# Kernel optimization log

Hardware: AMD Instinct MI355X
Metric: run time of the kernel (lower is better)

The kernel has to match this reference:

```python
import jax, jax.numpy as jnp
import numpy as np

EPS = 1e-5

def _layernorm(x, w, b):
    mu = jnp.mean(x, axis=-1, keepdims=True)
    var = jnp.mean(jnp.square(x - mu), axis=-1, keepdims=True)
    return (x - mu) * jax.lax.rsqrt(var + EPS) * w + b

def setup_inputs() -> dict:
    key = jax.random.key(0)
    ks = jax.random.split(key, 8)
    L, D, FF = 4096, 768, 3072
    s = 1.0 / np.sqrt(D)
    return {
        "x": jax.random.normal(ks[0], (L, D), jnp.float32),
        "in_proj_w": jax.random.normal(ks[1], (3 * D, D), jnp.float32) * s,
        "in_proj_b": jnp.zeros((3 * D,), jnp.float32),
        "out_w": jax.random.normal(ks[2], (D, D), jnp.float32) * s,
        "out_b": jnp.zeros((D,), jnp.float32),
        "ln1_w": jnp.ones((D,), jnp.float32),
        "ln1_b": jnp.zeros((D,), jnp.float32),
        "ln2_w": jnp.ones((D,), jnp.float32),
        "ln2_b": jnp.zeros((D,), jnp.float32),
        "ff_w1": jax.random.normal(ks[3], (FF, D), jnp.float32) * s,
        "ff_b1": jnp.zeros((FF,), jnp.float32),
        "ff_w2": jax.random.normal(ks[4], (D, FF), jnp.float32) * (1.0 / np.sqrt(FF)),
        "ff_b2": jnp.zeros((D,), jnp.float32),
        "window": 128,
    }

def reference(x, in_proj_w, in_proj_b, out_w, out_b, ln1_w, ln1_b, ln2_w, ln2_b, ff_w1, ff_b1, ff_w2, ff_b2, window):
    L, D = x.shape
    H = 12
    hd = D // H
    # packed qkv projection (torch MultiheadAttention in_proj)
    qkv = x @ in_proj_w.T + in_proj_b          # [L, 3D]
    q, k, v = jnp.split(qkv, 3, axis=-1)
    q = q.reshape(L, H, hd).transpose(1, 0, 2)  # [H, L, hd]
    k = k.reshape(L, H, hd).transpose(1, 0, 2)
    v = v.reshape(L, H, hd).transpose(1, 0, 2)
    scores = jnp.einsum('hqd,hkd->hqk', q, k) / np.sqrt(hd)  # [H, L, L]
    idx = jnp.arange(L)
    banned = jnp.abs(idx[:, None] - idx[None, :]) > window    # True = disallowed
    scores = jnp.where(banned[None], -jnp.inf, scores)
    probs = jax.nn.softmax(scores, axis=-1)
    ctx = jnp.einsum('hqk,hkd->hqd', probs, v)               # [H, L, hd]
    ctx = ctx.transpose(1, 0, 2).reshape(L, D)
    attn_out = ctx @ out_w.T + out_b
    h = _layernorm(x + attn_out, ln1_w, ln1_b)
    ff = jax.nn.gelu(h @ ff_w1.T + ff_b1, approximate=False) @ ff_w2.T + ff_b2
    return _layernorm(h + ff, ln2_w, ln2_b)
```

## Files before the change

kernel.cpp:

```cpp
#include <hip/hip_runtime.h>

typedef __bf16 bf16x8 __attribute__((ext_vector_type(8)));
typedef float f32x4 __attribute__((ext_vector_type(4)));

__device__ __forceinline__ unsigned short f2b(float f) {
    unsigned int u = __float_as_uint(f);
    u = (u + 0x7fffu + ((u >> 16) & 1u)) >> 16;
    return (unsigned short)u;
}

__global__ __launch_bounds__(256) void cvt_all(
    const float* __restrict__ s0, unsigned short* __restrict__ d0,
    const float* __restrict__ s1, unsigned short* __restrict__ d1,
    const float* __restrict__ s2, unsigned short* __restrict__ d2,
    const float* __restrict__ s3, unsigned short* __restrict__ d3,
    const float* __restrict__ s4, unsigned short* __restrict__ d4)
{
    int i = blockIdx.x * 256 + threadIdx.x;
    const float* s; unsigned short* d; int j;
    if (i < 786432)       { s = s0; d = d0; j = i; }
    else if (i < 1228800) { s = s1; d = d1; j = i - 786432; }
    else if (i < 1376256) { s = s2; d = d2; j = i - 1228800; }
    else if (i < 1966080) { s = s3; d = d3; j = i - 1376256; }
    else                  { s = s4; d = d4; j = i - 1966080; }
    float4 v = ((const float4*)s)[j];
    ushort4 o;
    o.x = f2b(v.x); o.y = f2b(v.y); o.z = f2b(v.z); o.w = f2b(v.w);
    ((ushort4*)d)[j] = o;
}

#define GL16(g, s) __builtin_amdgcn_global_load_lds( \
    (const __attribute__((address_space(1))) unsigned int*)(g), \
    (__attribute__((address_space(3))) unsigned int*)(s), 16, 0, 0)

template<int EPI>
__global__ __launch_bounds__(512) void gemm_nt_256(
    const unsigned short* __restrict__ A,
    const unsigned short* __restrict__ B,
    const float* __restrict__ bias,
    float* __restrict__ Cf, unsigned short* __restrict__ Cb,
    int M, int N, int K)
{
    __shared__ __align__(16) unsigned short As[256 * 64];
    __shared__ __align__(16) unsigned short Bs[256 * 64];
    const int nwg = gridDim.x * gridDim.y;
    const int lin = blockIdx.y * gridDim.x + blockIdx.x;
    const int qq = nwg >> 3;
    const int swz = (lin & 7) * qq + (lin >> 3);
    const int bx = swz % gridDim.x;
    const int by = swz / gridDim.x;

    const int tid = threadIdx.x;
    const int l = tid & 63;
    const int w = tid >> 6;
    const int wr = w >> 2, wc = w & 3;
    const long arow = (long)by * 256 + (tid >> 3);
    const long brow = (long)bx * 256 + (tid >> 3);
    const int kc = (((tid & 7) ^ ((tid >> 3) & 7)) << 3);
    const unsigned short* Ap = A + arow * K + kc;
    const unsigned short* Bp = B + brow * K + kc;

    const int kslice = K / gridDim.z;
    const int kbeg = blockIdx.z * kslice;
    const int kend = kbeg + kslice;

    f32x4 acc[8][4] = {};

    for (int k0 = kbeg; k0 < kend; k0 += 64) {
#pragma unroll
        for (int i = 0; i < 4; ++i) {
            GL16(Ap + k0 + (long)64 * i * K, As + i * 4096 + tid * 8);
            GL16(Bp + k0 + (long)64 * i * K, Bs + i * 4096 + tid * 8);
        }
        __syncthreads();
#pragma unroll
        for (int kk = 0; kk < 2; ++kk) {
            bf16x8 b[4];
#pragma unroll
            for (int n = 0; n < 4; ++n) {
                const int row = wc * 64 + n * 16 + (l & 15);
                const int ch = (kk * 4 + (l >> 4)) ^ (row & 7);
                b[n] = *(const bf16x8*)&Bs[row * 64 + (ch << 3)];
            }
#pragma unroll
            for (int m = 0; m < 8; ++m) {
                const int row = wr * 128 + m * 16 + (l & 15);
                const int ch = (kk * 4 + (l >> 4)) ^ (row & 7);
                bf16x8 a = *(const bf16x8*)&As[row * 64 + (ch << 3)];
#pragma unroll
                for (int n = 0; n < 4; ++n)
                    acc[m][n] = __builtin_amdgcn_mfma_f32_16x16x32_bf16(a, b[n], acc[m][n], 0, 0, 0);
            }
        }
        __syncthreads();
    }

    const int r0 = by * 256 + wr * 128 + ((l >> 4) << 2);
    const int c0 = bx * 256 + wc * 64 + (l & 15);
#pragma unroll
    for (int n = 0; n < 4; ++n) {
        const int col = c0 + n * 16;
        const float bv = (EPI == 3) ? 0.0f : bias[col];
#pragma unroll
        for (int m = 0; m < 8; ++m) {
#pragma unroll
            for (int r = 0; r < 4; ++r) {
                long row = r0 + m * 16 + r;
                float v = acc[m][n][r];
                if (EPI == 3) {
                    Cf[(long)blockIdx.z * M * N + row * N + col] = v;
                } else {
                    v += bv;
                    if (EPI == 2) v = 0.5f * v * (1.0f + erff(v * 0.70710678f));
                    Cb[row * N + col] = f2b(v);
                }
            }
        }
    }
}

template<int EPI>
__global__ __launch_bounds__(256) void gemm_nt(
    const unsigned short* __restrict__ A,
    const unsigned short* __restrict__ B,
    const float* __restrict__ bias,
    float* __restrict__ Cf, unsigned short* __restrict__ Cb,
    int M, int N, int K)
{
    __shared__ __align__(16) unsigned short As[128 * 64];
    __shared__ __align__(16) unsigned short Bs[128 * 64];
    const int nwg = gridDim.x * gridDim.y;
    const int lin = blockIdx.y * gridDim.x + blockIdx.x;
    const int qq = nwg >> 3;
    const int swz = (lin & 7) * qq + (lin >> 3);
    const int bx = swz % gridDim.x;
    const int by = swz / gridDim.x;

    const int tid = threadIdx.x;
    const int l = tid & 63;
    const int w = tid >> 6;
    const int wr = w >> 1, wc = w & 1;
    const long arow = (long)by * 128 + (tid >> 3);
    const long brow = (long)bx * 128 + (tid >> 3);
    const int kc = (tid & 7) * 8;
    const unsigned short* Ap = A + arow * K + kc;
    const unsigned short* Bp = B + brow * K + kc;

    const int kslice = K / gridDim.z;
    const int kbeg = blockIdx.z * kslice;
    const int kend = kbeg + kslice;

    f32x4 acc[4][4] = {};

    for (int k0 = kbeg; k0 < kend; k0 += 64) {
#pragma unroll
        for (int i = 0; i < 4; ++i) {
            GL16(Ap + k0 + (long)32 * i * K, As + i * 2048 + tid * 8);
            GL16(Bp + k0 + (long)32 * i * K, Bs + i * 2048 + tid * 8);
        }
        __syncthreads();
#pragma unroll
        for (int kk = 0; kk < 2; ++kk) {
            bf16x8 a[4], b[4];
#pragma unroll
            for (int m = 0; m < 4; ++m)
                a[m] = *(const bf16x8*)&As[(wr * 64 + m * 16 + (l & 15)) * 64 + kk * 32 + (l >> 4) * 8];
#pragma unroll
            for (int n = 0; n < 4; ++n)
                b[n] = *(const bf16x8*)&Bs[(wc * 64 + n * 16 + (l & 15)) * 64 + kk * 32 + (l >> 4) * 8];
#pragma unroll
            for (int m = 0; m < 4; ++m)
#pragma unroll
                for (int n = 0; n < 4; ++n)
                    acc[m][n] = __builtin_amdgcn_mfma_f32_16x16x32_bf16(a[m], b[n], acc[m][n], 0, 0, 0);
        }
        __syncthreads();
    }

    const int r0 = by * 128 + wr * 64 + ((l >> 4) << 2);
    const int c0 = bx * 128 + wc * 64 + (l & 15);
#pragma unroll
    for (int n = 0; n < 4; ++n) {
        const int col = c0 + n * 16;
        const float bv = (EPI == 3) ? 0.0f : bias[col];
#pragma unroll
        for (int m = 0; m < 4; ++m) {
#pragma unroll
            for (int r = 0; r < 4; ++r) {
                long row = r0 + m * 16 + r;
                float v = acc[m][n][r];
                if (EPI == 3) {
                    Cf[(long)blockIdx.z * M * N + row * N + col] = v;
                } else {
                    v += bv;
                    if (EPI == 2) v = 0.5f * v * (1.0f + erff(v * 0.70710678f));
                    if (EPI == 1) Cf[row * N + col] = v;
                    else          Cb[row * N + col] = f2b(v);
                }
            }
        }
    }
}

__global__ __launch_bounds__(256) void attn_local(
    const unsigned short* __restrict__ qkv,
    unsigned short* __restrict__ ctx,
    const int* __restrict__ winp)
{
    const int L = 4096;
    const int W = *winp;
    const int h = blockIdx.y;
    const int q0 = blockIdx.x * 64;
    const int tid = threadIdx.x;
    const int w = tid >> 6, l = tid & 63;
    __shared__ __align__(16) unsigned short Qs[64 * 64];
    __shared__ __align__(16) unsigned short Ks[64 * 64];
    __shared__ __align__(16) unsigned short Vs[64 * 64];
    __shared__ __align__(16) unsigned short Ps[64 * 64];

    {
        const int cg = tid & 7;
#pragma unroll
        for (int i = 0; i < 2; ++i) {
            int r = (tid >> 3) + 32 * i;
            uint4 v = *(const uint4*)&qkv[(long)(q0 + r) * 2304 + h * 64 + cg * 8];
            *(uint4*)&Qs[r * 64 + ((cg ^ (r & 7)) << 3)] = v;
        }
    }

    float mrow[4], lrow[4];
    f32x4 o[4] = {};
#pragma unroll
    for (int r = 0; r < 4; ++r) { mrow[r] = -1e30f; lrow[r] = 0.0f; }

    for (int st = 0; st < 5; ++st) {
        const int k0 = q0 - 128 + st * 64;
        __syncthreads();
        {
            const int cg = tid & 7;
#pragma unroll
            for (int i = 0; i < 2; ++i) {
                int r = (tid >> 3) + 32 * i;
                int kr = k0 + r;
                int krc = kr < 0 ? 0 : (kr >= L ? L - 1 : kr);
                uint4 kv = *(const uint4*)&qkv[(long)krc * 2304 + 768 + h * 64 + cg * 8];
                *(uint4*)&Ks[r * 64 + ((cg ^ (r & 7)) << 3)] = kv;
                uint4 vv = *(const uint4*)&qkv[(long)krc * 2304 + 1536 + h * 64 + cg * 8];
#pragma unroll
                for (int jj = 0; jj < 4; ++jj) {
                    unsigned int word = (jj == 0) ? vv.x : (jj == 1) ? vv.y : (jj == 2) ? vv.z : vv.w;
                    int d0 = cg * 8 + jj * 2;
                    int d1 = d0 + 1;
                    Vs[d0 * 64 + (((r >> 3) ^ (d0 & 7)) << 3) + (r & 7)] = (unsigned short)(word & 0xffffu);
                    Vs[d1 * 64 + (((r >> 3) ^ (d1 & 7)) << 3) + (r & 7)] = (unsigned short)(word >> 16);
                }
            }
        }
        __syncthreads();

        f32x4 s[4] = {};
#pragma unroll
        for (int kk = 0; kk < 2; ++kk) {
            const int aro = w * 16 + (l & 15);
            bf16x8 aq = *(const bf16x8*)&Qs[aro * 64 + (((kk * 4 + (l >> 4)) ^ (aro & 7)) << 3)];
#pragma unroll
            for (int n = 0; n < 4; ++n) {
                const int bro = n * 16 + (l & 15);
                bf16x8 bk = *(const bf16x8*)&Ks[bro * 64 + (((kk * 4 + (l >> 4)) ^ (bro & 7)) << 3)];
                s[n] = __builtin_amdgcn_mfma_f32_16x16x32_bf16(aq, bk, s[n], 0, 0, 0);
            }
        }

        const int qrow = q0 + w * 16 + ((l >> 4) << 2);
        const int kcol = k0 + (l & 15);
        float p[4][4];
#pragma unroll
        for (int n = 0; n < 4; ++n) {
#pragma unroll
            for (int r = 0; r < 4; ++r) {
                int key = kcol + n * 16;
                int q = qrow + r;
                int dd = q - key; if (dd < 0) dd = -dd;
                bool banned = (key < 0) || (key >= L) || (dd > W);
                p[n][r] = banned ? -1e30f : s[n][r] * 0.125f;
            }
        }
        float mx[4];
#pragma unroll
        for (int r = 0; r < 4; ++r)
            mx[r] = fmaxf(fmaxf(p[0][r], p[1][r]), fmaxf(p[2][r], p[3][r]));
#pragma unroll
        for (int off = 8; off >= 1; off >>= 1)
#pragma unroll
            for (int r = 0; r < 4; ++r)
                mx[r] = fmaxf(mx[r], __shfl_xor(mx[r], off));

        float sc[4], mn[4];
#pragma unroll
        for (int r = 0; r < 4; ++r) {
            mn[r] = fmaxf(mrow[r], mx[r]);
            sc[r] = __expf(mrow[r] - mn[r]);
            mrow[r] = mn[r];
        }
        float rs[4] = {0.f, 0.f, 0.f, 0.f};
#pragma unroll
        for (int n = 0; n < 4; ++n)
#pragma unroll
            for (int r = 0; r < 4; ++r) {
                float pv = __expf(p[n][r] - mn[r]);
                p[n][r] = pv;
                rs[r] += pv;
            }
#pragma unroll
        for (int off = 8; off >= 1; off >>= 1)
#pragma unroll
            for (int r = 0; r < 4; ++r)
                rs[r] += __shfl_xor(rs[r], off);
#pragma unroll
        for (int r = 0; r < 4; ++r)
            lrow[r] = lrow[r] * sc[r] + rs[r];
#pragma unroll
        for (int n = 0; n < 4; ++n)
#pragma unroll
            for (int r = 0; r < 4; ++r)
                o[n][r] *= sc[r];

#pragma unroll
        for (int n = 0; n < 4; ++n) {
            int col = n * 16 + (l & 15);
            int cb = col >> 3, ci = col & 7;
#pragma unroll
            for (int r = 0; r < 4; ++r) {
                int rp = w * 16 + ((l >> 4) << 2) + r;
                Ps[rp * 64 + ((cb ^ (rp & 7)) << 3) + ci] = f2b(p[n][r]);
            }
        }
#pragma unroll
        for (int kk = 0; kk < 2; ++kk) {
            const int aro = w * 16 + (l & 15);
            bf16x8 ap = *(const bf16x8*)&Ps[aro * 64 + (((kk * 4 + (l >> 4)) ^ (aro & 7)) << 3)];
#pragma unroll
            for (int n = 0; n < 4; ++n) {
                const int bro = n * 16 + (l & 15);
                bf16x8 bv = *(const bf16x8*)&Vs[bro * 64 + (((kk * 4 + (l >> 4)) ^ (bro & 7)) << 3)];
                o[n] = __builtin_amdgcn_mfma_f32_16x16x32_bf16(ap, bv, o[n], 0, 0, 0);
            }
        }
    }

#pragma unroll
    for (int n = 0; n < 4; ++n) {
        int col = h * 64 + n * 16 + (l & 15);
#pragma unroll
        for (int r = 0; r < 4; ++r) {
            int q = q0 + w * 16 + ((l >> 4) << 2) + r;
            ctx[(long)q * 768 + col] = f2b(o[n][r] / lrow[r]);
        }
    }
}

__global__ __launch_bounds__(256) void ln_res2(
    const float* __restrict__ A, const float* __restrict__ parts,
    const float* __restrict__ pbias,
    const float* __restrict__ w, const float* __restrict__ bb,
    float* __restrict__ outf, unsigned short* __restrict__ outb)
{
    const int D = 768;
    const long PS = (long)4096 * 768;
    const int row = blockIdx.x;
    const int t = threadIdx.x;
    const long base = (long)row * D;
    float xs[3];
#pragma unroll
    for (int i = 0; i < 3; ++i) {
        int c = t + i * 256;
        xs[i] = A[base + c] + pbias[c] + parts[base + c] + parts[PS + base + c];
    }
    float s = xs[0] + xs[1] + xs[2];
    float ss = xs[0] * xs[0] + xs[1] * xs[1] + xs[2] * xs[2];
#pragma unroll
    for (int off = 32; off >= 1; off >>= 1) {
        s += __shfl_xor(s, off);
        ss += __shfl_xor(ss, off);
    }
    __shared__ float sm[8];
    if ((t & 63) == 0) { sm[t >> 6] = s; sm[(t >> 6) + 4] = ss; }
    __syncthreads();
    s = sm[0] + sm[1] + sm[2] + sm[3];
    ss = sm[4] + sm[5] + sm[6] + sm[7];
    float mu = s * (1.0f / 768.0f);
    float var = ss * (1.0f / 768.0f) - mu * mu;
    float rstd = rsqrtf(var + 1e-5f);
#pragma unroll
    for (int i = 0; i < 3; ++i) {
        int c = t + i * 256;
        float y = (xs[i] - mu) * rstd * w[c] + bb[c];
        outf[base + c] = y;
        if (outb) outb[base + c] = f2b(y);
    }
}

extern "C" void kernel_launch(void* const* d_in, const int* in_sizes, int n_in,
                              void* d_out, int out_size, void* d_ws, size_t ws_size,
                              hipStream_t stream) {
    const float* x   = (const float*)d_in[0];
    const float* ipw = (const float*)d_in[1];
    const float* ipb = (const float*)d_in[2];
    const float* ow  = (const float*)d_in[3];
    const float* ob  = (const float*)d_in[4];
    const float* l1w = (const float*)d_in[5];
    const float* l1b = (const float*)d_in[6];
    const float* l2w = (const float*)d_in[7];
    const float* l2b = (const float*)d_in[8];
    const float* fw1 = (const float*)d_in[9];
    const float* fb1 = (const float*)d_in[10];
    const float* fw2 = (const float*)d_in[11];
    const float* fb2 = (const float*)d_in[12];
    const int*   win = (const int*)d_in[13];

    const int L = 4096, D = 768, TD = 2304, FF = 3072;
    char* p = (char*)d_ws;
    unsigned short* xb   = (unsigned short*)p; p += (size_t)L * D * 2;
    unsigned short* wqkv = (unsigned short*)p; p += (size_t)TD * D * 2;
    unsigned short* wout = (unsigned short*)p; p += (size_t)D * D * 2;
    unsigned short* wf1  = (unsigned short*)p; p += (size_t)FF * D * 2;
    unsigned short* wf2  = (unsigned short*)p; p += (size_t)FF * D * 2;
    unsigned short* ctxb = (unsigned short*)p; p += (size_t)L * D * 2;
    float* parts         = (float*)p;          p += (size_t)2 * L * D * 4;
    float* hf            = (float*)p;          p += (size_t)L * D * 4;
    unsigned short* big  = (unsigned short*)p; p += (size_t)L * FF * 2;
    unsigned short* qkvb = big;
    unsigned short* gb   = big;
    unsigned short* hb   = ctxb;

    cvt_all<<<9984, 256, 0, stream>>>(x, xb, ipw, wqkv, ow, wout, fw1, wf1, fw2, wf2);

    gemm_nt_256<0><<<dim3(TD / 256, L / 256, 1), 512, 0, stream>>>(xb, wqkv, ipb, nullptr, qkvb, L, TD, D);
    attn_local<<<dim3(L / 64, 12), 256, 0, stream>>>(qkvb, ctxb, win);
    gemm_nt<3><<<dim3(D / 128, L / 128, 2), 256, 0, stream>>>(ctxb, wout, nullptr, parts, nullptr, L, D, D);
    ln_res2<<<L, 256, 0, stream>>>(x, parts, ob, l1w, l1b, hf, hb);
    gemm_nt_256<2><<<dim3(FF / 256, L / 256, 1), 512, 0, stream>>>(hb, wf1, fb1, nullptr, gb, L, FF, D);
    gemm_nt_256<3><<<dim3(D / 256, L / 256, 2), 512, 0, stream>>>(gb, wf2, nullptr, parts, nullptr, L, D, FF);
    ln_res2<<<L, 256, 0, stream>>>(hf, parts, fb2, l2w, l2b, (float*)d_out, nullptr);
}
```

Measured before the change: 314.8 us.

## Double-buffer GEMM LDS tiles and store FF2 split-K partials as bf16 with 4 slices

Both GEMM kernels gain double-buffered LDS tiles, so the global-to-LDS loads for the next K tile are issued before computing the current one, overlapping memory with MFMA work. The 256-tile kernel drops its XOR swizzle in the LDS layout, which may bring back bank conflicts. The second FFN GEMM now splits K four ways and writes bf16 partials, which the templated residual+LayerNorm kernel sums. This raises parallelism and cuts partial-sum traffic, but loses precision in the partial sums and doubles LDS use, which can lower occupancy.

New measurement: 305.3 us. 1.03x faster.

```diff
diff --git a/kernel.cpp b/kernel.cpp
--- a/kernel.cpp
+++ b/kernel.cpp
@@ -7,6 +7,9 @@
     unsigned int u = __float_as_uint(f);
     u = (u + 0x7fffu + ((u >> 16) & 1u)) >> 16;
     return (unsigned short)u;
+}
+__device__ __forceinline__ float b2f(unsigned short v) {
+    return __uint_as_float(((unsigned int)v) << 16);
 }
 
 __global__ __launch_bounds__(256) void cvt_all(
@@ -34,15 +37,15 @@
     (__attribute__((address_space(3))) unsigned int*)(s), 16, 0, 0)
 
 template<int EPI>
-__global__ __launch_bounds__(512) void gemm_nt_256(
+__global__ __launch_bounds__(512) void gemm256(
     const unsigned short* __restrict__ A,
     const unsigned short* __restrict__ B,
     const float* __restrict__ bias,
-    float* __restrict__ Cf, unsigned short* __restrict__ Cb,
+    unsigned short* __restrict__ Cb,
     int M, int N, int K)
 {
-    __shared__ __align__(16) unsigned short As[256 * 64];
-    __shared__ __align__(16) unsigned short Bs[256 * 64];
+    __shared__ __align__(16) unsigned short As[2][256 * 64];
+    __shared__ __align__(16) unsigned short Bs[2][256 * 64];
     const int nwg = gridDim.x * gridDim.y;
     const int lin = blockIdx.y * gridDim.x + blockIdx.x;
     const int qq = nwg >> 3;
@@ -56,43 +59,49 @@
     const int wr = w >> 2, wc = w & 3;
     const long arow = (long)by * 256 + (tid >> 3);
     const long brow = (long)bx * 256 + (tid >> 3);
-    const int kc = (((tid & 7) ^ ((tid >> 3) & 7)) << 3);
+    const int kc = (tid & 7) * 8;
     const unsigned short* Ap = A + arow * K + kc;
     const unsigned short* Bp = B + brow * K + kc;
 
     const int kslice = K / gridDim.z;
     const int kbeg = blockIdx.z * kslice;
-    const int kend = kbeg + kslice;
+    const int nt = kslice >> 6;
 
     f32x4 acc[8][4] = {};
 
-    for (int k0 = kbeg; k0 < kend; k0 += 64) {
-#pragma unroll
-        for (int i = 0; i < 4; ++i) {
-            GL16(Ap + k0 + (long)64 * i * K, As + i * 4096 + tid * 8);
-            GL16(Bp + k0 + (long)64 * i * K, Bs + i * 4096 + tid * 8);
-        }
-        __syncthreads();
+#pragma unroll
+    for (int i = 0; i < 4; ++i) {
+        GL16(Ap + kbeg + (long)64 * i * K, &As[0][i * 4096 + tid * 8]);
+        GL16(Bp + kbeg + (long)64 * i * K, &Bs[0][i * 4096 + tid * 8]);
+    }
+    __syncthreads();
+
+    int cur = 0;
+    for (int t = 0; t < nt; ++t) {
+        if (t + 1 < nt) {
+            const long k0 = kbeg + (long)(t + 1) * 64;
+#pragma unroll
+            for (int i = 0; i < 4; ++i) {
+                GL16(Ap + k0 + (long)64 * i * K, &As[cur ^ 1][i * 4096 + tid * 8]);
+                GL16(Bp + k0 + (long)64 * i * K, &Bs[cur ^ 1][i * 4096 + tid * 8]);
+            }
+        }
 #pragma unroll
         for (int kk = 0; kk < 2; ++kk) {
             bf16x8 b[4];
 #pragma unroll
-            for (int n = 0; n < 4; ++n) {
-                const int row = wc * 64 + n * 16 + (l & 15);
-                const int ch = (kk * 4 + (l >> 4)) ^ (row & 7);
-                b[n] = *(const bf16x8*)&Bs[row * 64 + (ch << 3)];
-            }
+            for (int n = 0; n < 4; ++n)
+                b[n] = *(const bf16x8*)&Bs[cur][(wc * 64 + n * 16 + (l & 15)) * 64 + kk * 32 + (l >> 4) * 8];
 #pragma unroll
             for (int m = 0; m < 8; ++m) {
-                const int row = wr * 128 + m * 16 + (l & 15);
-                const int ch = (kk * 4 + (l >> 4)) ^ (row & 7);
-                bf16x8 a = *(const bf16x8*)&As[row * 64 + (ch << 3)];
+                bf16x8 a = *(const bf16x8*)&As[cur][(wr * 128 + m * 16 + (l & 15)) * 64 + kk * 32 + (l >> 4) * 8];
 #pragma unroll
                 for (int n = 0; n < 4; ++n)
                     acc[m][n] = __builtin_amdgcn_mfma_f32_16x16x32_bf16(a, b[n], acc[m][n], 0, 0, 0);
             }
         }
         __syncthreads();
+        cur ^= 1;
     }
 
     const int r0 = by * 256 + wr * 128 + ((l >> 4) << 2);
@@ -100,15 +109,15 @@
 #pragma unroll
     for (int n = 0; n < 4; ++n) {
         const int col = c0 + n * 16;
-        const float bv = (EPI == 3) ? 0.0f : bias[col];
+        const float bv = (EPI == 4) ? 0.0f : bias[col];
 #pragma unroll
         for (int m = 0; m < 8; ++m) {
 #pragma unroll
             for (int r = 0; r < 4; ++r) {
                 long row = r0 + m * 16 + r;
                 float v = acc[m][n][r];
-                if (EPI == 3) {
-                    Cf[(long)blockIdx.z * M * N + row * N + col] = v;
+                if (EPI == 4) {
+                    Cb[(long)blockIdx.z * M * N + row * N + col] = f2b(v);
                 } else {
                     v += bv;
                     if (EPI == 2) v = 0.5f * v * (1.0f + erff(v * 0.70710678f));
@@ -120,15 +129,14 @@
 }
 
 template<int EPI>
-__global__ __launch_bounds__(256) void gemm_nt(
+__global__ __launch_bounds__(256) void gemm_nt_p(
     const unsigned short* __restrict__ A,
     const unsigned short* __restrict__ B,
-    const float* __restrict__ bias,
-    float* __restrict__ Cf, unsigned short* __restrict__ Cb,
+    float* __restrict__ Cf,
     int M, int N, int K)
 {
-    __shared__ __align__(16) unsigned short As[128 * 64];
-    __shared__ __align__(16) unsigned short Bs[128 * 64];
+    __shared__ __align__(16) unsigned short As[2][128 * 64];
+    __shared__ __align__(16) unsigned short Bs[2][128 * 64];
     const int nwg = gridDim.x * gridDim.y;
     const int lin = blockIdx.y * gridDim.x + blockIdx.x;
     const int qq = nwg >> 3;
@@ -148,26 +156,36 @@
 
     const int kslice = K / gridDim.z;
     const int kbeg = blockIdx.z * kslice;
-    const int kend = kbeg + kslice;
+    const int nt = kslice >> 6;
 
     f32x4 acc[4][4] = {};
 
-    for (int k0 = kbeg; k0 < kend; k0 += 64) {
-#pragma unroll
-        for (int i = 0; i < 4; ++i) {
-            GL16(Ap + k0 + (long)32 * i * K, As + i * 2048 + tid * 8);
-            GL16(Bp + k0 + (long)32 * i * K, Bs + i * 2048 + tid * 8);
-        }
-        __syncthreads();
+#pragma unroll
+    for (int i = 0; i < 4; ++i) {
+        GL16(Ap + kbeg + (long)32 * i * K, &As[0][i * 2048 + tid * 8]);
+        GL16(Bp + kbeg + (long)32 * i * K, &Bs[0][i * 2048 + tid * 8]);
+    }
+    __syncthreads();
+
+    int cur = 0;
+    for (int t = 0; t < nt; ++t) {
+        if (t + 1 < nt) {
+            const long k0 = kbeg + (long)(t + 1) * 64;
+#pragma unroll
+            for (int i = 0; i < 4; ++i) {
+                GL16(Ap + k0 + (long)32 * i * K, &As[cur ^ 1][i * 2048 + tid * 8]);
+                GL16(Bp + k0 + (long)32 * i * K, &Bs[cur ^ 1][i * 2048 + tid * 8]);
+            }
+        }
 #pragma unroll
         for (int kk = 0; kk < 2; ++kk) {
             bf16x8 a[4], b[4];
 #pragma unroll
             for (int m = 0; m < 4; ++m)
-                a[m] = *(const bf16x8*)&As[(wr * 64 + m * 16 + (l & 15)) * 64 + kk * 32 + (l >> 4) * 8];
+                a[m] = *(const bf16x8*)&As[cur][(wr * 64 + m * 16 + (l & 15)) * 64 + kk * 32 + (l >> 4) * 8];
 #pragma unroll
             for (int n = 0; n < 4; ++n)
-                b[n] = *(const bf16x8*)&Bs[(wc * 64 + n * 16 + (l & 15)) * 64 + kk * 32 + (l >> 4) * 8];
+                b[n] = *(const bf16x8*)&Bs[cur][(wc * 64 + n * 16 + (l & 15)) * 64 + kk * 32 + (l >> 4) * 8];
 #pragma unroll
             for (int m = 0; m < 4; ++m)
 #pragma unroll
@@ -175,6 +193,7 @@
                     acc[m][n] = __builtin_amdgcn_mfma_f32_16x16x32_bf16(a[m], b[n], acc[m][n], 0, 0, 0);
         }
         __syncthreads();
+        cur ^= 1;
     }
 
     const int r0 = by * 128 + wr * 64 + ((l >> 4) << 2);
@@ -182,21 +201,12 @@
 #pragma unroll
     for (int n = 0; n < 4; ++n) {
         const int col = c0 + n * 16;
-        const float bv = (EPI == 3) ? 0.0f : bias[col];
 #pragma unroll
         for (int m = 0; m < 4; ++m) {
 #pragma unroll
             for (int r = 0; r < 4; ++r) {
                 long row = r0 + m * 16 + r;
-                float v = acc[m][n][r];
-                if (EPI == 3) {
-                    Cf[(long)blockIdx.z * M * N + row * N + col] = v;
-                } else {
-                    v += bv;
-                    if (EPI == 2) v = 0.5f * v * (1.0f + erff(v * 0.70710678f));
-                    if (EPI == 1) Cf[row * N + col] = v;
-                    else          Cb[row * N + col] = f2b(v);
-                }
+                Cf[(long)blockIdx.z * M * N + row * N + col] = acc[m][n][r];
             }
         }
     }
@@ -359,8 +369,9 @@
     }
 }
 
+template<int NS, int BF>
 __global__ __launch_bounds__(256) void ln_res2(
-    const float* __restrict__ A, const float* __restrict__ parts,
+    const float* __restrict__ A, const void* __restrict__ partsv,
     const float* __restrict__ pbias,
     const float* __restrict__ w, const float* __restrict__ bb,
     float* __restrict__ outf, unsigned short* __restrict__ outb)
@@ -374,7 +385,17 @@
 #pragma unroll
     for (int i = 0; i < 3; ++i) {
         int c = t + i * 256;
-        xs[i] = A[base + c] + pbias[c] + parts[base + c] + parts[PS + base + c];
+        float v = A[base + c] + pbias[c];
+        if (BF) {
+            const unsigned short* pb = (const unsigned short*)partsv;
+#pragma unroll
+            for (int s = 0; s < NS; ++s) v += b2f(pb[s * PS + base + c]);
+        } else {
+            const float* pf = (const float*)partsv;
+#pragma unroll
+            for (int s = 0; s < NS; ++s) v += pf[s * PS + base + c];
+        }
+        xs[i] = v;
     }
     float s = xs[0] + xs[1] + xs[2];
     float ss = xs[0] * xs[0] + xs[1] * xs[1] + xs[2] * xs[2];
@@ -426,20 +447,22 @@
     unsigned short* wf1  = (unsigned short*)p; p += (size_t)FF * D * 2;
     unsigned short* wf2  = (unsigned short*)p; p += (size_t)FF * D * 2;
     unsigned short* ctxb = (unsigned short*)p; p += (size_t)L * D * 2;
-    float* parts         = (float*)p;          p += (size_t)2 * L * D * 4;
+    char* partsRaw       = p;                  p += (size_t)2 * L * D * 4;
     float* hf            = (float*)p;          p += (size_t)L * D * 4;
     unsigned short* big  = (unsigned short*)p; p += (size_t)L * FF * 2;
     unsigned short* qkvb = big;
     unsigned short* gb   = big;
     unsigned short* hb   = ctxb;
+    float* partsF        = (float*)partsRaw;
+    unsigned short* partsB = (unsigned short*)partsRaw;
 
     cvt_all<<<9984, 256, 0, stream>>>(x, xb, ipw, wqkv, ow, wout, fw1, wf1, fw2, wf2);
 
-    gemm_nt_256<0><<<dim3(TD / 256, L / 256, 1), 512, 0, stream>>>(xb, wqkv, ipb, nullptr, qkvb, L, TD, D);
+    gemm256<0><<<dim3(TD / 256, L / 256, 1), 512, 0, stream>>>(xb, wqkv, ipb, qkvb, L, TD, D);
     attn_local<<<dim3(L / 64, 12), 256, 0, stream>>>(qkvb, ctxb, win);
-    gemm_nt<3><<<dim3(D / 128, L / 128, 2), 256, 0, stream>>>(ctxb, wout, nullptr, parts, nullptr, L, D, D);
-    ln_res2<<<L, 256, 0, stream>>>(x, parts, ob, l1w, l1b, hf, hb);
-    gemm_nt_256<2><<<dim3(FF / 256, L / 256, 1), 512, 0, stream>>>(hb, wf1, fb1, nullptr, gb, L, FF, D);
-    gemm_nt_256<3><<<dim3(D / 256, L / 256, 2), 512, 0, stream>>>(gb, wf2, nullptr, parts, nullptr, L, D, FF);
-    ln_res2<<<L, 256, 0, stream>>>(hf, parts, fb2, l2w, l2b, (float*)d_out, nullptr);
-}
+    gemm_nt_p<3><<<dim3(D / 128, L / 128, 2), 256, 0, stream>>>(ctxb, wout, partsF, L, D, D);
+    ln_res2<2, 0><<<L, 256, 0, stream>>>(x, partsF, ob, l1w, l1b, hf, hb);
+    gemm256<2><<<dim3(FF / 256, L / 256, 1), 512, 0, stream>>>(hb, wf1, fb1, gb, L, FF, D);
+    gemm256<4><<<dim3(D / 256, L / 256, 4), 512, 0, stream>>>(gb, wf2, nullptr, partsB, L, D, FF);
+    ln_res2<4, 1><<<L, 256, 0, stream>>>(hf, partsB, fb2, l2w, l2b, (float*)d_out, nullptr);
+}
```
